# Kernel tuning notes

Measured on AMD Instinct MI355X. Metric: run time of the kernel, lower is better.

The kernel has to match this reference:

```python
import jax, jax.numpy as jnp
import numpy as np

TREE_DEPTH = 6
IN_F, OUT_F = 1024, 1024
BATCH = 2048
N_LEAVES = 2 ** TREE_DEPTH
N_NODES = N_LEAVES - 1


def _tree_routes(depth):
    """Static routing table: for each leaf, the decision-node index visited at
    each depth and whether the leaf takes the sigmoid (1) or 1-sigmoid (0) branch.
    Mirrors the torch traversal: node = 2*node + 1 + bit; bits of leaf id LSB-first."""
    n_leaves = 2 ** depth
    idx = np.zeros((n_leaves, depth), dtype=np.int32)
    pos = np.zeros((n_leaves, depth), dtype=bool)
    for l in range(n_leaves):
        node, index = 0, l
        for d in range(depth):
            idx[l, d] = node
            pos[l, d] = (index % 2 == 0)
            node = node * 2 + 1 + index % 2
            index >>= 1
    return idx, pos

ROUTE_IDX, ROUTE_POS = _tree_routes(TREE_DEPTH)


def setup_inputs() -> dict:
    key = jax.random.key(0)
    kx, kwd, kwl = jax.random.split(key, 3)
    scale = 0.02  # keep sigmoid/softmax logits in a sane range
    x = jax.random.normal(kx, (BATCH, IN_F), dtype=jnp.float32)
    Wd = jax.random.normal(kwd, (N_NODES, IN_F), dtype=jnp.float32) * scale
    bd = jnp.zeros((N_NODES,), dtype=jnp.float32)
    Wl = jax.random.normal(kwl, (N_LEAVES, OUT_F, IN_F), dtype=jnp.float32) * scale
    bl = jnp.zeros((N_LEAVES, OUT_F), dtype=jnp.float32)
    return {"x": x, "Wd": Wd, "bd": bd, "Wl": Wl, "bl": bl}


def reference(x, Wd, bd, Wl, bl):
    # All decision node probabilities in one GEMM: [B, n_nodes]
    dprob = jax.nn.sigmoid(x @ Wd.T + bd)
    # Gather per-leaf path probs [B, L, depth] and take path product -> routing [B, L]
    path = dprob[:, ROUTE_IDX]                      # [B, L, D]
    path = jnp.where(ROUTE_POS, path, 1.0 - path)
    routing = jnp.prod(path, axis=-1)               # [B, L]
    # All leaf experts in one batched GEMM: [B, L, out], softmax over out (torch dim=1)
    leaf_logits = jnp.einsum('bi,loi->blo', x, Wl) + bl
    leaves = jax.nn.softmax(leaf_logits, axis=-1)
    # Routing-weighted sum over leaves
    return jnp.einsum('bl,blo->bo', routing, leaves)
```

## Files before the change

### kernel.cpp

```cpp
#include <hip/hip_runtime.h>
#include <hip/hip_bf16.h>

#define BATCH 2048
#define KD 1024
#define ND 1024
#define NLEAF 64
#define BM 256
#define BN 256

typedef __attribute__((ext_vector_type(8))) short bf16x8;
typedef __attribute__((ext_vector_type(4))) float f32x4;
typedef __attribute__((ext_vector_type(4))) _Float16 f16x4;

#define WLB_OFF 0ULL
#define XB_OFF  134217728ULL
#define RT_OFF  138412032ULL
#define LG_OFF  138936320ULL

__device__ __forceinline__ unsigned short f2bf(float f) {
  unsigned int u = __float_as_uint(f);
  u += 0x7fffu + ((u >> 16) & 1u);
  return (unsigned short)(u >> 16);
}

__device__ __forceinline__ void gload_lds16(const void* g, void* l) {
  __builtin_amdgcn_global_load_lds(
      (const __attribute__((address_space(1))) unsigned int*)g,
      (__attribute__((address_space(3))) unsigned int*)l, 16, 0, 0);
}

__global__ void __launch_bounds__(256) convert_kernel(
    const float* __restrict__ Wl, const float* __restrict__ x,
    unsigned short* __restrict__ wlb, unsigned short* __restrict__ xb) {
  const long long WL4 = 16777216LL;
  const long long X4  = 524288LL;
  long long i = (long long)blockIdx.x * 256 + threadIdx.x;
  const long long stride = (long long)gridDim.x * 256;
  for (; i < WL4 + X4; i += stride) {
    float4 v;
    if (i < WL4) v = ((const float4*)Wl)[i];
    else         v = ((const float4*)x)[i - WL4];
    ushort4 o;
    o.x = f2bf(v.x); o.y = f2bf(v.y); o.z = f2bf(v.z); o.w = f2bf(v.w);
    if (i < WL4) ((ushort4*)wlb)[i] = o;
    else         ((ushort4*)xb)[i - WL4] = o;
  }
}

__global__ void __launch_bounds__(256) routing_kernel(
    const float* __restrict__ x, const float* __restrict__ Wd,
    const float* __restrict__ bd, float* __restrict__ rt) {
  __shared__ float xs[4][KD];
  __shared__ float sdp[4][64];
  const int tid = threadIdx.x;
  const int b0 = blockIdx.x * 4;
  const float4* xsrc = (const float4*)(x + (size_t)b0 * KD);
  float4* xdst = (float4*)&xs[0][0];
  for (int i = tid; i < KD; i += 256) xdst[i] = xsrc[i];
  __syncthreads();
  const int wv = tid >> 6, ln = tid & 63;
  const int b = b0 + wv;
  if (ln < 63) {
    const float4* wrow = (const float4*)(Wd + (size_t)ln * KD);
    const float4* xr = (const float4*)&xs[wv][0];
    float4 a = {0.f, 0.f, 0.f, 0.f};
    for (int k = 0; k < KD / 4; ++k) {
      float4 w = wrow[k], xv = xr[k];
      a.x += w.x * xv.x; a.y += w.y * xv.y; a.z += w.z * xv.z; a.w += w.w * xv.w;
    }
    float z = a.x + a.y + a.z + a.w + bd[ln];
    sdp[wv][ln] = 1.f / (1.f + __expf(-z));
  }
  __syncthreads();
  float prod = 1.f;
  int node = 0, index = ln;
  for (int d = 0; d < 6; ++d) {
    float pv = sdp[wv][node];
    prod *= (index & 1) ? (1.f - pv) : pv;
    node = node * 2 + 1 + (index & 1);
    index >>= 1;
  }
  rt[(size_t)b * NLEAF + ln] = prod;
}

#define GBODY(CURA, CURB, NXTA, NXTB, S, VMASM, DOREAD)                      \
  {                                                                          \
    if ((S) + 3 < 32) STAGE((S) + 3);                                        \
    asm volatile(VMASM ::: "memory");                                        \
    asm volatile("s_waitcnt lgkmcnt(0)" ::: "memory");                       \
    asm volatile("s_barrier" ::: "memory");                                  \
    if (DOREAD) {                                                            \
      const char* nbuf = smem + (((S) + 1) & 3) * 32768;                     \
      _Pragma("unroll")                                                      \
      for (int mi = 0; mi < 8; ++mi)                                         \
        NXTA[mi] = *(const bf16x8*)(nbuf + offA[mi]);                        \
      _Pragma("unroll")                                                      \
      for (int ni = 0; ni < 4; ++ni)                                         \
        NXTB[ni] = *(const bf16x8*)(nbuf + 16384 + offB[ni]);                \
    }                                                                        \
    __builtin_amdgcn_sched_barrier(0);                                       \
    __builtin_amdgcn_s_setprio(1);                                           \
    _Pragma("unroll")                                                        \
    for (int mi = 0; mi < 8; ++mi)                                           \
      _Pragma("unroll")                                                      \
      for (int ni = 0; ni < 4; ++ni)                                         \
        acc[mi][ni] = __builtin_amdgcn_mfma_f32_16x16x32_bf16(               \
            CURA[mi], CURB[ni], acc[mi][ni], 0, 0, 0);                       \
    __builtin_amdgcn_s_setprio(0);                                           \
    __builtin_amdgcn_sched_barrier(0);                                       \
  }

__global__ void __launch_bounds__(512, 2) gemm_kernel(
    const unsigned short* __restrict__ A, const unsigned short* __restrict__ B,
    _Float16* __restrict__ C, int ntile) {
  extern __shared__ char smem[];
  const int tid = threadIdx.x;
  const int w = tid >> 6, ln = tid & 63;
  const int wm = w >> 2, wn = w & 3;
  const int g = ln >> 4, r16 = ln & 15;
  const int bid = blockIdx.x;
  const int j = bid >> 3;
  const int bm = (j & 7) * BM;
  const int bn = (((j >> 3) << 3) + (bid & 7)) * BN;
  const long long ldc = (long long)ntile * 256;

  const int rS = tid >> 2;
  const int cS = tid & 3;
  const int csrc = cS ^ ((rS >> 1) & 3);
  const unsigned short* ga0 = A + (size_t)(bm + rS) * KD + csrc * 8;
  const unsigned short* ga1 = ga0 + (size_t)128 * KD;
  const unsigned short* gb0 = B + (size_t)(bn + rS) * KD + csrc * 8;
  const unsigned short* gb1 = gb0 + (size_t)128 * KD;
  const int ldsw = w * 1024;

  auto STAGE = [&](int t) {
    char* base = smem + (t & 3) * 32768;
    const size_t ko = (size_t)t * 32;
    gload_lds16(ga0 + ko, base + ldsw);
    gload_lds16(ga1 + ko, base + 8192 + ldsw);
    gload_lds16(gb0 + ko, base + 16384 + ldsw);
    gload_lds16(gb1 + ko, base + 24576 + ldsw);
  };

  int offA[8], offB[4];
#pragma unroll
  for (int mi = 0; mi < 8; ++mi) {
    const int row = wm * 128 + mi * 16 + r16;
    offA[mi] = row * 64 + (g ^ ((row >> 1) & 3)) * 16;
  }
#pragma unroll
  for (int ni = 0; ni < 4; ++ni) {
    const int row = wn * 64 + ni * 16 + r16;
    offB[ni] = row * 64 + (g ^ ((row >> 1) & 3)) * 16;
  }

  f32x4 acc[8][4];
#pragma unroll
  for (int mi = 0; mi < 8; ++mi)
#pragma unroll
    for (int ni = 0; ni < 4; ++ni) acc[mi][ni] = (f32x4){0.f, 0.f, 0.f, 0.f};

  bf16x8 aE[8], bE[4], aO[8], bO[4];

  STAGE(0); STAGE(1); STAGE(2);
  asm volatile("s_waitcnt vmcnt(8)" ::: "memory");
  asm volatile("s_barrier" ::: "memory");
  {
    const char* nbuf = smem;
#pragma unroll
    for (int mi = 0; mi < 8; ++mi) aE[mi] = *(const bf16x8*)(nbuf + offA[mi]);
#pragma unroll
    for (int ni = 0; ni < 4; ++ni) bE[ni] = *(const bf16x8*)(nbuf + 16384 + offB[ni]);
  }

  for (int u = 0; u < 14; ++u) {
    GBODY(aE, bE, aO, bO, 2 * u,     "s_waitcnt vmcnt(8)", 1);
    GBODY(aO, bO, aE, bE, 2 * u + 1, "s_waitcnt vmcnt(8)", 1);
  }
  GBODY(aE, bE, aO, bO, 28, "s_waitcnt vmcnt(8)", 1);
  GBODY(aO, bO, aE, bE, 29, "s_waitcnt vmcnt(4)", 1);
  GBODY(aE, bE, aO, bO, 30, "s_waitcnt vmcnt(0)", 1);
  GBODY(aO, bO, aE, bE, 31, "s_waitcnt vmcnt(0)", 0);

#pragma unroll
  for (int mi = 0; mi < 8; ++mi)
#pragma unroll
    for (int q = 0; q < 4; ++q) {
      const long long grow = bm + wm * 128 + mi * 16 + g * 4 + q;
#pragma unroll
      for (int ni = 0; ni < 4; ++ni) {
        const int gcol = bn + wn * 64 + ni * 16 + r16;
        C[grow * ldc + gcol] = (_Float16)acc[mi][ni][q];
      }
    }
}

__global__ void __launch_bounds__(256) smax_kernel(
    const _Float16* __restrict__ Cg, const float* __restrict__ rt,
    const float* __restrict__ bl, float* __restrict__ out,
    int lpg, int l0, int first) {
  __shared__ float reds[2][2][4];
  __shared__ float rts[64];
  const int tid = threadIdx.x;
  const int b = blockIdx.x;
  const int w = tid >> 6, ln = tid & 63;
  const int c0 = tid * 4;
  if (tid < lpg) rts[tid] = rt[(size_t)b * NLEAF + l0 + tid];
  __syncthreads();
  float oacc[4] = {0.f, 0.f, 0.f, 0.f};
  const long long ldc = (long long)lpg * ND;

  for (int jj = 0; jj < lpg; jj += 2) {
    const int par = (jj >> 1) & 1;
    const f16x4 h0 = *(const f16x4*)(Cg + (size_t)b * ldc + jj * ND + c0);
    const f16x4 h1 = *(const f16x4*)(Cg + (size_t)b * ldc + (jj + 1) * ND + c0);
    const float4 bv0 = *(const float4*)(bl + (size_t)(l0 + jj) * ND + c0);
    const float4 bv1 = *(const float4*)(bl + (size_t)(l0 + jj + 1) * ND + c0);
    float e0[4], e1[4], s0 = 0.f, s1 = 0.f;
    e0[0] = __expf((float)h0[0] + bv0.x); e0[1] = __expf((float)h0[1] + bv0.y);
    e0[2] = __expf((float)h0[2] + bv0.z); e0[3] = __expf((float)h0[3] + bv0.w);
    e1[0] = __expf((float)h1[0] + bv1.x); e1[1] = __expf((float)h1[1] + bv1.y);
    e1[2] = __expf((float)h1[2] + bv1.z); e1[3] = __expf((float)h1[3] + bv1.w);
#pragma unroll
    for (int k = 0; k < 4; ++k) { s0 += e0[k]; s1 += e1[k]; }
#pragma unroll
    for (int off = 1; off < 64; off <<= 1) {
      s0 += __shfl_xor(s0, off);
      s1 += __shfl_xor(s1, off);
    }
    if (ln == 0) { reds[par][0][w] = s0; reds[par][1][w] = s1; }
    __syncthreads();
    const float S0 = reds[par][0][0] + reds[par][0][1] + reds[par][0][2] + reds[par][0][3];
    const float S1 = reds[par][1][0] + reds[par][1][1] + reds[par][1][2] + reds[par][1][3];
    const float c0f = rts[jj] / S0;
    const float c1f = rts[jj + 1] / S1;
#pragma unroll
    for (int k = 0; k < 4; ++k) oacc[k] += c0f * e0[k] + c1f * e1[k];
  }

  float* orow = out + (size_t)b * ND + c0;
  if (first) {
    *(float4*)orow = (float4){oacc[0], oacc[1], oacc[2], oacc[3]};
  } else {
    float4 p = *(const float4*)orow;
    p.x += oacc[0]; p.y += oacc[1]; p.z += oacc[2]; p.w += oacc[3];
    *(float4*)orow = p;
  }
}

extern "C" void kernel_launch(void* const* d_in, const int* in_sizes, int n_in,
                              void* d_out, int out_size, void* d_ws, size_t ws_size,
                              hipStream_t stream) {
  const float* x  = (const float*)d_in[0];
  const float* Wd = (const float*)d_in[1];
  const float* bd = (const float*)d_in[2];
  const float* Wl = (const float*)d_in[3];
  const float* bl = (const float*)d_in[4];
  float* out = (float*)d_out;
  char* ws = (char*)d_ws;
  unsigned short* wlb = (unsigned short*)(ws + WLB_OFF);
  unsigned short* xb  = (unsigned short*)(ws + XB_OFF);
  float* rt           = (float*)(ws + RT_OFF);
  _Float16* lg        = (_Float16*)(ws + LG_OFF);

  convert_kernel<<<2048, 256, 0, stream>>>(Wl, x, wlb, xb);
  routing_kernel<<<BATCH / 4, 256, 0, stream>>>(x, Wd, bd, rt);
  hipFuncSetAttribute((const void*)gemm_kernel,
                      hipFuncAttributeMaxDynamicSharedMemorySize, 131072);

  const int ngrp = (ws_size >= LG_OFF + (size_t)BATCH * NLEAF * ND * 2) ? 1 : 4;
  const int lpg = NLEAF / ngrp;
  const int ntile = lpg * (ND / BN);
  for (int grp = 0; grp < ngrp; ++grp) {
    gemm_kernel<<<8 * ntile, 512, 131072, stream>>>(
        xb, wlb + (size_t)grp * lpg * ND * KD, lg, ntile);
    smax_kernel<<<BATCH, 256, 0, stream>>>(lg, rt, bl, out,
                                           lpg, grp * lpg, grp == 0);
  }
}
```

Before: 501.6 us.

## Fuse leaf bias into GEMM epilogue, wave-per-row softmax, interleave LDS reads with MFMA

The leaf bias add moves into the GEMM epilogue, so the softmax kernel no longer loads the bias tensor. The softmax kernel is restructured so each wavefront owns one batch row. Reductions then use only shuffles, which removes the per-leaf __syncthreads and LDS reductions, and loads become 16-byte. The GEMM main loop also adds sched_group_barrier hints that interleave the next-stage LDS reads with MFMAs and raise priority earlier, to hide LDS latency.

```diff
diff --git a/kernel.cpp b/kernel.cpp
--- a/kernel.cpp
+++ b/kernel.cpp
@@ -10,7 +10,7 @@
 
 typedef __attribute__((ext_vector_type(8))) short bf16x8;
 typedef __attribute__((ext_vector_type(4))) float f32x4;
-typedef __attribute__((ext_vector_type(4))) _Float16 f16x4;
+typedef __attribute__((ext_vector_type(8))) _Float16 f16x8;
 
 #define WLB_OFF 0ULL
 #define XB_OFF  134217728ULL
@@ -88,7 +88,9 @@
     if ((S) + 3 < 32) STAGE((S) + 3);                                        \
     asm volatile(VMASM ::: "memory");                                        \
     asm volatile("s_waitcnt lgkmcnt(0)" ::: "memory");                       \
+    __builtin_amdgcn_sched_barrier(0);                                       \
     asm volatile("s_barrier" ::: "memory");                                  \
+    __builtin_amdgcn_s_setprio(1);                                           \
     if (DOREAD) {                                                            \
       const char* nbuf = smem + (((S) + 1) & 3) * 32768;                     \
       _Pragma("unroll")                                                      \
@@ -98,21 +100,27 @@
       for (int ni = 0; ni < 4; ++ni)                                         \
         NXTB[ni] = *(const bf16x8*)(nbuf + 16384 + offB[ni]);                \
     }                                                                        \
-    __builtin_amdgcn_sched_barrier(0);                                       \
-    __builtin_amdgcn_s_setprio(1);                                           \
     _Pragma("unroll")                                                        \
     for (int mi = 0; mi < 8; ++mi)                                           \
       _Pragma("unroll")                                                      \
       for (int ni = 0; ni < 4; ++ni)                                         \
         acc[mi][ni] = __builtin_amdgcn_mfma_f32_16x16x32_bf16(               \
             CURA[mi], CURB[ni], acc[mi][ni], 0, 0, 0);                       \
+    if (DOREAD) {                                                            \
+      _Pragma("unroll")                                                      \
+      for (int r = 0; r < 12; ++r) {                                         \
+        __builtin_amdgcn_sched_group_barrier(0x100, 1, 0);    \
+        __builtin_amdgcn_sched_group_barrier(0x008, 2, 0);    \
+      }                                                                      \
+      __builtin_amdgcn_sched_group_barrier(0x008, 8, 0);      \
+    }                                                                        \
     __builtin_amdgcn_s_setprio(0);                                           \
     __builtin_amdgcn_sched_barrier(0);                                       \
   }
 
 __global__ void __launch_bounds__(512, 2) gemm_kernel(
     const unsigned short* __restrict__ A, const unsigned short* __restrict__ B,
-    _Float16* __restrict__ C, int ntile) {
+    const float* __restrict__ blg, _Float16* __restrict__ C, int ntile) {
   extern __shared__ char smem[];
   const int tid = threadIdx.x;
   const int w = tid >> 6, ln = tid & 63;
@@ -182,6 +190,11 @@
   GBODY(aE, bE, aO, bO, 30, "s_waitcnt vmcnt(0)", 1);
   GBODY(aO, bO, aE, bE, 31, "s_waitcnt vmcnt(0)", 0);
 
+  const int lf = bn >> 10;
+  float blv[4];
+#pragma unroll
+  for (int ni = 0; ni < 4; ++ni)
+    blv[ni] = blg[(size_t)lf * ND + (bn & 1023) + wn * 64 + ni * 16 + r16];
 #pragma unroll
   for (int mi = 0; mi < 8; ++mi)
 #pragma unroll
@@ -190,61 +203,55 @@
 #pragma unroll
       for (int ni = 0; ni < 4; ++ni) {
         const int gcol = bn + wn * 64 + ni * 16 + r16;
-        C[grow * ldc + gcol] = (_Float16)acc[mi][ni][q];
+        C[grow * ldc + gcol] = (_Float16)(acc[mi][ni][q] + blv[ni]);
       }
     }
 }
 
 __global__ void __launch_bounds__(256) smax_kernel(
     const _Float16* __restrict__ Cg, const float* __restrict__ rt,
-    const float* __restrict__ bl, float* __restrict__ out,
-    int lpg, int l0, int first) {
-  __shared__ float reds[2][2][4];
-  __shared__ float rts[64];
+    float* __restrict__ out, int lpg, int l0, int first) {
   const int tid = threadIdx.x;
-  const int b = blockIdx.x;
-  const int w = tid >> 6, ln = tid & 63;
-  const int c0 = tid * 4;
-  if (tid < lpg) rts[tid] = rt[(size_t)b * NLEAF + l0 + tid];
-  __syncthreads();
-  float oacc[4] = {0.f, 0.f, 0.f, 0.f};
+  const int wv = tid >> 6, ln = tid & 63;
+  const int b = blockIdx.x * 4 + wv;
   const long long ldc = (long long)lpg * ND;
-
-  for (int jj = 0; jj < lpg; jj += 2) {
-    const int par = (jj >> 1) & 1;
-    const f16x4 h0 = *(const f16x4*)(Cg + (size_t)b * ldc + jj * ND + c0);
-    const f16x4 h1 = *(const f16x4*)(Cg + (size_t)b * ldc + (jj + 1) * ND + c0);
-    const float4 bv0 = *(const float4*)(bl + (size_t)(l0 + jj) * ND + c0);
-    const float4 bv1 = *(const float4*)(bl + (size_t)(l0 + jj + 1) * ND + c0);
-    float e0[4], e1[4], s0 = 0.f, s1 = 0.f;
-    e0[0] = __expf((float)h0[0] + bv0.x); e0[1] = __expf((float)h0[1] + bv0.y);
-    e0[2] = __expf((float)h0[2] + bv0.z); e0[3] = __expf((float)h0[3] + bv0.w);
-    e1[0] = __expf((float)h1[0] + bv1.x); e1[1] = __expf((float)h1[1] + bv1.y);
-    e1[2] = __expf((float)h1[2] + bv1.z); e1[3] = __expf((float)h1[3] + bv1.w);
-#pragma unroll
-    for (int k = 0; k < 4; ++k) { s0 += e0[k]; s1 += e1[k]; }
-#pragma unroll
-    for (int off = 1; off < 64; off <<= 1) {
-      s0 += __shfl_xor(s0, off);
-      s1 += __shfl_xor(s1, off);
+  const _Float16* base = Cg + (size_t)b * ldc + ln * 8;
+  const float rtv = (ln < lpg) ? rt[(size_t)b * NLEAF + l0 + ln] : 0.f;
+
+  float oacc[16];
+#pragma unroll
+  for (int k = 0; k < 16; ++k) oacc[k] = 0.f;
+
+  for (int jj = 0; jj < lpg; ++jj) {
+    const f16x8 h0 = *(const f16x8*)(base + jj * ND);
+    const f16x8 h1 = *(const f16x8*)(base + jj * ND + 512);
+    float e[16], s = 0.f;
+#pragma unroll
+    for (int k = 0; k < 8; ++k) { e[k] = __expf((float)h0[k]); s += e[k]; }
+#pragma unroll
+    for (int k = 0; k < 8; ++k) { e[8 + k] = __expf((float)h1[k]); s += e[8 + k]; }
+#pragma unroll
+    for (int off = 1; off < 64; off <<= 1) s += __shfl_xor(s, off);
+    const float coef = __shfl(rtv, jj) / s;
+#pragma unroll
+    for (int k = 0; k < 16; ++k) oacc[k] += coef * e[k];
+  }
+
+  float* o0 = out + (size_t)b * ND + ln * 8;
+  if (first) {
+    *(float4*)o0         = (float4){oacc[0], oacc[1], oacc[2], oacc[3]};
+    *(float4*)(o0 + 4)   = (float4){oacc[4], oacc[5], oacc[6], oacc[7]};
+    *(float4*)(o0 + 512) = (float4){oacc[8], oacc[9], oacc[10], oacc[11]};
+    *(float4*)(o0 + 516) = (float4){oacc[12], oacc[13], oacc[14], oacc[15]};
+  } else {
+#pragma unroll
+    for (int part = 0; part < 4; ++part) {
+      float* p = o0 + (part >> 1) * 512 + (part & 1) * 4;
+      float4 v = *(const float4*)p;
+      v.x += oacc[part * 4 + 0]; v.y += oacc[part * 4 + 1];
+      v.z += oacc[part * 4 + 2]; v.w += oacc[part * 4 + 3];
+      *(float4*)p = v;
     }
-    if (ln == 0) { reds[par][0][w] = s0; reds[par][1][w] = s1; }
-    __syncthreads();
-    const float S0 = reds[par][0][0] + reds[par][0][1] + reds[par][0][2] + reds[par][0][3];
-    const float S1 = reds[par][1][0] + reds[par][1][1] + reds[par][1][2] + reds[par][1][3];
-    const float c0f = rts[jj] / S0;
-    const float c1f = rts[jj + 1] / S1;
-#pragma unroll
-    for (int k = 0; k < 4; ++k) oacc[k] += c0f * e0[k] + c1f * e1[k];
-  }
-
-  float* orow = out + (size_t)b * ND + c0;
-  if (first) {
-    *(float4*)orow = (float4){oacc[0], oacc[1], oacc[2], oacc[3]};
-  } else {
-    float4 p = *(const float4*)orow;
-    p.x += oacc[0]; p.y += oacc[1]; p.z += oacc[2]; p.w += oacc[3];
-    *(float4*)orow = p;
   }
 }
 
@@ -273,8 +280,9 @@
   const int ntile = lpg * (ND / BN);
   for (int grp = 0; grp < ngrp; ++grp) {
     gemm_kernel<<<8 * ntile, 512, 131072, stream>>>(
-        xb, wlb + (size_t)grp * lpg * ND * KD, lg, ntile);
-    smax_kernel<<<BATCH, 256, 0, stream>>>(lg, rt, bl, out,
-                                           lpg, grp * lpg, grp == 0);
-  }
-}
+        xb, wlb + (size_t)grp * lpg * ND * KD,
+        bl + (size_t)grp * lpg * ND, lg, ntile);
+    smax_kernel<<<BATCH / 4, 256, 0, stream>>>(lg, rt, out,
+                                               lpg, grp * lpg, grp == 0);
+  }
+}
```

After: 498.0 us. Within noise of the previous version (-0.7%).
